# Performance work log

Measured on AMD Instinct MI355X. Metric: run time of the kernel, lower is better.

Reference implementation:

```python
import jax, jax.numpy as jnp
import numpy as np

HIDDEN = 51
INPUT = 1
OUTPUT = 1
BATCH = 4096
SEQ = 999


def setup_inputs() -> dict:
    key = jax.random.key(0)
    ks = jax.random.split(key, 7)
    s = 1.0 / np.sqrt(HIDDEN)  # PyTorch default LSTM/Linear init scale
    u = lambda k, shape: jax.random.uniform(k, shape, jnp.float32, -s, s)
    return {
        "input": jax.random.normal(ks[0], (BATCH, SEQ, INPUT), jnp.float32),
        "W_ih": u(ks[1], (4 * HIDDEN, INPUT)),
        "W_hh": u(ks[2], (4 * HIDDEN, HIDDEN)),
        "b_ih": u(ks[3], (4 * HIDDEN,)),
        "b_hh": u(ks[4], (4 * HIDDEN,)),
        "W_fc": u(ks[5], (OUTPUT, HIDDEN)),
        "b_fc": u(ks[6], (OUTPUT,)),
        "future": 0,
    }


def reference(input, W_ih, W_hh, b_ih, b_hh, W_fc, b_fc, future):
    # Single-layer LSTM (PyTorch gate order i, f, g, o) scanned over time,
    # followed by a per-timestep Linear -> (batch, seq+future, output).
    def step(carry, x_t):
        h, c = carry
        gates = x_t @ W_ih.T + b_ih + h @ W_hh.T + b_hh  # (B, 4H)
        i, f, g, o = jnp.split(gates, 4, axis=-1)
        c = jax.nn.sigmoid(f) * c + jax.nn.sigmoid(i) * jnp.tanh(g)
        h = jax.nn.sigmoid(o) * jnp.tanh(c)
        return (h, c), h

    B = input.shape[0]
    h0 = jnp.zeros((B, HIDDEN), input.dtype)
    c0 = jnp.zeros((B, HIDDEN), input.dtype)
    xs = jnp.swapaxes(input, 0, 1)  # (T, B, I)
    (h, c), hs = jax.lax.scan(step, (h0, c0), xs)
    ys = hs @ W_fc.T + b_fc  # (T, B, O)

    # static Python int, so a trace-time loop is fine).
    y = ys[-1]
    extra = []
    for _ in range(future):
        (h, c), hn = step((h, c), y)
        y = hn @ W_fc.T + b_fc
        extra.append(y)
    if extra:
        ys = jnp.concatenate([ys, jnp.stack(extra, 0)], axis=0)
    return jnp.swapaxes(ys, 0, 1)  # (B, T+future, O)
```

## Files before the change

kernel.cpp:

```cpp
#include <hip/hip_runtime.h>
#include <hip/hip_bf16.h>

#define HID   51
#define MR    208
#define SEQT  999
#define CH    111
#define NCH   9
#define EPB   16
#define XST   17
#define NTH   448
#define BSTR  72

typedef __attribute__((ext_vector_type(8))) short  short8;
typedef __attribute__((ext_vector_type(4))) float  floatx4;

__global__ void prep_kernel(const float* __restrict__ W_hh,
                            const float* __restrict__ W_ih,
                            const float* __restrict__ W_fc,
                            __hip_bfloat16* __restrict__ A_ext)
{
    const float K1 = 1.442695040889f;
    int idx = blockIdx.x * blockDim.x + threadIdx.x;
    if (idx >= MR * 64) return;
    int r = idx >> 6, k = idx & 63;
    int u = r >> 2, gate = r & 3;
    float v = 0.f;
    if (r == 204) {
        if (k < HID) v = W_fc[k];
    } else if (u < HID) {
        float s = (gate == 2) ? (-2.f * K1) : (-K1);
        if (k < HID)      v = s * W_hh[(gate * HID + u) * HID + k];
        else if (k == 51) v = s * W_ih[gate * HID + u];
    }
    A_ext[idx] = __float2bfloat16(v);
}

__launch_bounds__(NTH)
__global__ void lstm_mfma_kernel(const float* __restrict__ x,
                                 const float* __restrict__ b_ih,
                                 const float* __restrict__ b_hh,
                                 const float* __restrict__ b_fc,
                                 const __hip_bfloat16* __restrict__ A_ext,
                                 float* __restrict__ out)
{
    __shared__ __hip_bfloat16 bcol[2][16 * BSTR];
    __shared__ float x_lds[(CH + 1) * XST];
    __shared__ float y_lds[CH * XST];

    const int tid  = threadIdx.x;
    const int w    = tid >> 6;
    const int lane = tid & 63;
    const int e    = lane & 15;
    const int g4   = lane >> 4;
    const int e0   = blockIdx.x * EPB;
    const bool w6  = (w == 6);
    const int  uB6   = 48 + g4;
    const bool yln   = w6 && (g4 == 3);
    const bool xsv   = w6 && (g4 == 0);
    const int  wrow6 = (uB6 < HID) ? uB6 : 63;

    const float K1  = 1.442695040889f;
    const float K2N = -2.885390081777f;

    short8  A0a = {0,0,0,0,0,0,0,0}, A1a = {0,0,0,0,0,0,0,0};
    short8  A0b = {0,0,0,0,0,0,0,0}, A1b = {0,0,0,0,0,0,0,0};
    floatx4 bqa = {0.f, 0.f, 0.f, 0.f}, bqb = {0.f, 0.f, 0.f, 0.f};
    float   csa = 0.f, csb = 0.f;
    int ua = 0, ub = 0;

    if (!w6) {
        int Ta = 2 * w, Tb = 2 * w + 1;
        ua = 4 * Ta + g4; ub = 4 * Tb + g4;
        int ma = Ta * 16 + e, mb = Tb * 16 + e;
        A0a = *(const short8*)&A_ext[ma * 64 + g4 * 8];
        A1a = *(const short8*)&A_ext[ma * 64 + 32 + g4 * 8];
        A0b = *(const short8*)&A_ext[mb * 64 + g4 * 8];
        A1b = *(const short8*)&A_ext[mb * 64 + 32 + g4 * 8];
#pragma unroll
        for (int gg = 0; gg < 4; ++gg) {
            float s = (gg == 2) ? (-2.f * K1) : (-K1);
            bqa[gg] = s * (b_ih[gg * HID + ua] + b_hh[gg * HID + ua]);
            bqb[gg] = s * (b_ih[gg * HID + ub] + b_hh[gg * HID + ub]);
        }
    } else {
        int m = 12 * 16 + e;
        A0a = *(const short8*)&A_ext[m * 64 + g4 * 8];
        A1a = *(const short8*)&A_ext[m * 64 + 32 + g4 * 8];
        if (uB6 < HID) {
#pragma unroll
            for (int gg = 0; gg < 4; ++gg) {
                float s = (gg == 2) ? (-2.f * K1) : (-K1);
                bqa[gg] = s * (b_ih[gg * HID + uB6] + b_hh[gg * HID + uB6]);
            }
        }
    }

    for (int i = tid; i < 16 * BSTR; i += NTH) {
        bcol[0][i] = __float2bfloat16(0.f);
        bcol[1][i] = __float2bfloat16(0.f);
    }
    __syncthreads();
    if (tid < EPB)
        bcol[0][tid * BSTR + 51] = __float2bfloat16(x[(size_t)(e0 + tid) * SEQT]);
    const float bfc = b_fc[0];

    __syncthreads();

    for (int tc = 0; tc < NCH; ++tc) {
        const int t0 = tc * CH;
        for (int i2 = tid; i2 < (CH + 1) * EPB; i2 += NTH) {
            int ee = i2 / (CH + 1), tt = i2 % (CH + 1);
            int t = t0 + tt;
            x_lds[tt * XST + ee] = (t < SEQT) ? x[(size_t)(e0 + ee) * SEQT + t] : 0.f;
        }
        __syncthreads();

        for (int tt = 0; tt < CH; ++tt) {
            const int t  = t0 + tt;
            const int rp = t & 1, wp = rp ^ 1;

            short8 B0 = *(const short8*)&bcol[rp][e * BSTR + g4 * 8];
            short8 B1 = *(const short8*)&bcol[rp][e * BSTR + 32 + g4 * 8];

            if (!w6) {
                floatx4 aa = __builtin_amdgcn_mfma_f32_16x16x32_bf16(A0a, B0, bqa, 0, 0, 0);
                floatx4 ab = __builtin_amdgcn_mfma_f32_16x16x32_bf16(A0b, B0, bqb, 0, 0, 0);
                aa = __builtin_amdgcn_mfma_f32_16x16x32_bf16(A1a, B1, aa, 0, 0, 0);
                ab = __builtin_amdgcn_mfma_f32_16x16x32_bf16(A1b, B1, ab, 0, 0, 0);

                float Eia = __builtin_amdgcn_exp2f(aa[0]);
                float Efa = __builtin_amdgcn_exp2f(aa[1]);
                float Ega = __builtin_amdgcn_exp2f(aa[2]);
                float Eoa = __builtin_amdgcn_exp2f(aa[3]);
                float Eib = __builtin_amdgcn_exp2f(ab[0]);
                float Efb = __builtin_amdgcn_exp2f(ab[1]);
                float Egb = __builtin_amdgcn_exp2f(ab[2]);
                float Eob = __builtin_amdgcn_exp2f(ab[3]);

                float sfa  = __builtin_amdgcn_rcpf(1.f + Efa);
                float sfb  = __builtin_amdgcn_rcpf(1.f + Efb);
                float Riga = __builtin_amdgcn_rcpf(fmaf(Eia, Ega, (Eia + Ega) + 1.f));
                float Rigb = __builtin_amdgcn_rcpf(fmaf(Eib, Egb, (Eib + Egb) + 1.f));
                csa = fmaf(sfa, csa, K2N * ((1.f - Ega) * Riga));
                csb = fmaf(sfb, csb, K2N * ((1.f - Egb) * Rigb));
                float Eca = __builtin_amdgcn_exp2f(csa);
                float Ecb = __builtin_amdgcn_exp2f(csb);
                float Roca = __builtin_amdgcn_rcpf(fmaf(Eoa, Eca, (Eoa + Eca) + 1.f));
                float Rocb = __builtin_amdgcn_rcpf(fmaf(Eob, Ecb, (Eob + Ecb) + 1.f));
                float ha = (1.f - Eca) * Roca;
                float hb = (1.f - Ecb) * Rocb;

                bcol[wp][e * BSTR + ua] = __float2bfloat16(ha);
                bcol[wp][e * BSTR + ub] = __float2bfloat16(hb);
            } else {
                floatx4 acc = __builtin_amdgcn_mfma_f32_16x16x32_bf16(A0a, B0, bqa, 0, 0, 0);
                acc = __builtin_amdgcn_mfma_f32_16x16x32_bf16(A1a, B1, acc, 0, 0, 0);

                float Ei = __builtin_amdgcn_exp2f(acc[0]);
                float Ef = __builtin_amdgcn_exp2f(acc[1]);
                float Eg = __builtin_amdgcn_exp2f(acc[2]);
                float Eo = __builtin_amdgcn_exp2f(acc[3]);
                float sf  = __builtin_amdgcn_rcpf(1.f + Ef);
                float Rig = __builtin_amdgcn_rcpf(fmaf(Ei, Eg, (Ei + Eg) + 1.f));
                csa = fmaf(sf, csa, K2N * ((1.f - Eg) * Rig));
                float Ec = __builtin_amdgcn_exp2f(csa);
                float Roc = __builtin_amdgcn_rcpf(fmaf(Eo, Ec, (Eo + Ec) + 1.f));
                float h = (1.f - Ec) * Roc;

                bcol[wp][e * BSTR + wrow6] = __float2bfloat16((uB6 < HID) ? h : 0.f);
                if (yln) y_lds[tt * XST + e] = acc[0] + bfc;
                if (xsv) bcol[wp][e * BSTR + 51] =
                             __float2bfloat16(x_lds[(tt + 1) * XST + e]);
            }

            __syncthreads();
        }
        __syncthreads();

        for (int i2 = tid; i2 < CH * EPB; i2 += NTH) {
            int ee = i2 / CH, tt = i2 % CH;
            int t = t0 + tt - 1;
            if (t >= 0)
                out[(size_t)(e0 + ee) * SEQT + t] = y_lds[tt * XST + ee];
        }
        __syncthreads();
    }

    if (w6) {
        short8 B0 = *(const short8*)&bcol[1][e * BSTR + g4 * 8];
        short8 B1 = *(const short8*)&bcol[1][e * BSTR + 32 + g4 * 8];
        floatx4 acc = __builtin_amdgcn_mfma_f32_16x16x32_bf16(A0a, B0, bqa, 0, 0, 0);
        acc = __builtin_amdgcn_mfma_f32_16x16x32_bf16(A1a, B1, acc, 0, 0, 0);
        if (g4 == 3)
            out[(size_t)(e0 + e) * SEQT + (SEQT - 1)] = acc[0] + bfc;
    }
}

extern "C" void kernel_launch(void* const* d_in, const int* in_sizes, int n_in,
                              void* d_out, int out_size, void* d_ws, size_t ws_size,
                              hipStream_t stream) {
    const float* x    = (const float*)d_in[0];
    const float* W_ih = (const float*)d_in[1];
    const float* W_hh = (const float*)d_in[2];
    const float* b_ih = (const float*)d_in[3];
    const float* b_hh = (const float*)d_in[4];
    const float* W_fc = (const float*)d_in[5];
    const float* b_fc = (const float*)d_in[6];
    float* out = (float*)d_out;

    __hip_bfloat16* A_ext = (__hip_bfloat16*)d_ws;

    prep_kernel<<<(MR * 64 + 255) / 256, 256, 0, stream>>>(W_hh, W_ih, W_fc, A_ext);
    lstm_mfma_kernel<<<4096 / EPB, NTH, 0, stream>>>(x, b_ih, b_hh,
                                                     b_fc, A_ext, out);
}
```

Baseline: 435.1 us.

## Spread gate tiles over 13 waves, one tile each, and merge cell-update reciprocals

Each block now runs 13 waves of one 16-row MFMA tile each, instead of 7 waves where 6 handled two tiles, so every wave executes identical code and the per-step serial chain per wave is shorter. The cell update is rewritten algebraically so the forget and input/gate reciprocals become a single reciprocal of their product. The aim is a shorter per-timestep critical path in this latency-bound recurrence. In exchange there are more waves per block, more costly barriers, and possibly fewer blocks resident per CU.

Result: slower. 498.5 us (+14.6%).

```diff
diff --git a/kernel.cpp b/kernel.cpp
--- a/kernel.cpp
+++ b/kernel.cpp
@@ -8,7 +8,7 @@
 #define NCH   9
 #define EPB   16
 #define XST   17
-#define NTH   448
+#define NTH   832
 #define BSTR  72
 
 typedef __attribute__((ext_vector_type(8))) short  short8;
@@ -53,45 +53,29 @@
     const int e    = lane & 15;
     const int g4   = lane >> 4;
     const int e0   = blockIdx.x * EPB;
-    const bool w6  = (w == 6);
-    const int  uB6   = 48 + g4;
-    const bool yln   = w6 && (g4 == 3);
-    const bool xsv   = w6 && (g4 == 0);
-    const int  wrow6 = (uB6 < HID) ? uB6 : 63;
+
+    const int  u    = 4 * w + g4;
+    const bool yln  = (u == 51);
+    const bool xsv  = (w == 12) && (g4 == 0);
+    const int  wrow = (u < HID) ? u : 63;
 
     const float K1  = 1.442695040889f;
     const float K2N = -2.885390081777f;
 
-    short8  A0a = {0,0,0,0,0,0,0,0}, A1a = {0,0,0,0,0,0,0,0};
-    short8  A0b = {0,0,0,0,0,0,0,0}, A1b = {0,0,0,0,0,0,0,0};
-    floatx4 bqa = {0.f, 0.f, 0.f, 0.f}, bqb = {0.f, 0.f, 0.f, 0.f};
-    float   csa = 0.f, csb = 0.f;
-    int ua = 0, ub = 0;
+    short8  A0, A1;
+    floatx4 bq = {0.f, 0.f, 0.f, 0.f};
+    float   cs = 0.f;
 
-    if (!w6) {
-        int Ta = 2 * w, Tb = 2 * w + 1;
-        ua = 4 * Ta + g4; ub = 4 * Tb + g4;
-        int ma = Ta * 16 + e, mb = Tb * 16 + e;
-        A0a = *(const short8*)&A_ext[ma * 64 + g4 * 8];
-        A1a = *(const short8*)&A_ext[ma * 64 + 32 + g4 * 8];
-        A0b = *(const short8*)&A_ext[mb * 64 + g4 * 8];
-        A1b = *(const short8*)&A_ext[mb * 64 + 32 + g4 * 8];
+    {
+        int m = w * 16 + e;
+        A0 = *(const short8*)&A_ext[m * 64 + g4 * 8];
+        A1 = *(const short8*)&A_ext[m * 64 + 32 + g4 * 8];
+    }
+    if (u < HID) {
 #pragma unroll
         for (int gg = 0; gg < 4; ++gg) {
             float s = (gg == 2) ? (-2.f * K1) : (-K1);
-            bqa[gg] = s * (b_ih[gg * HID + ua] + b_hh[gg * HID + ua]);
-            bqb[gg] = s * (b_ih[gg * HID + ub] + b_hh[gg * HID + ub]);
-        }
-    } else {
-        int m = 12 * 16 + e;
-        A0a = *(const short8*)&A_ext[m * 64 + g4 * 8];
-        A1a = *(const short8*)&A_ext[m * 64 + 32 + g4 * 8];
-        if (uB6 < HID) {
-#pragma unroll
-            for (int gg = 0; gg < 4; ++gg) {
-                float s = (gg == 2) ? (-2.f * K1) : (-K1);
-                bqa[gg] = s * (b_ih[gg * HID + uB6] + b_hh[gg * HID + uB6]);
-            }
+            bq[gg] = s * (b_ih[gg * HID + u] + b_hh[gg * HID + u]);
         }
     }
 
@@ -122,56 +106,27 @@
             short8 B0 = *(const short8*)&bcol[rp][e * BSTR + g4 * 8];
             short8 B1 = *(const short8*)&bcol[rp][e * BSTR + 32 + g4 * 8];
 
-            if (!w6) {
-                floatx4 aa = __builtin_amdgcn_mfma_f32_16x16x32_bf16(A0a, B0, bqa, 0, 0, 0);
-                floatx4 ab = __builtin_amdgcn_mfma_f32_16x16x32_bf16(A0b, B0, bqb, 0, 0, 0);
-                aa = __builtin_amdgcn_mfma_f32_16x16x32_bf16(A1a, B1, aa, 0, 0, 0);
-                ab = __builtin_amdgcn_mfma_f32_16x16x32_bf16(A1b, B1, ab, 0, 0, 0);
+            floatx4 acc = __builtin_amdgcn_mfma_f32_16x16x32_bf16(A0, B0, bq, 0, 0, 0);
+            acc = __builtin_amdgcn_mfma_f32_16x16x32_bf16(A1, B1, acc, 0, 0, 0);
 
-                float Eia = __builtin_amdgcn_exp2f(aa[0]);
-                float Efa = __builtin_amdgcn_exp2f(aa[1]);
-                float Ega = __builtin_amdgcn_exp2f(aa[2]);
-                float Eoa = __builtin_amdgcn_exp2f(aa[3]);
-                float Eib = __builtin_amdgcn_exp2f(ab[0]);
-                float Efb = __builtin_amdgcn_exp2f(ab[1]);
-                float Egb = __builtin_amdgcn_exp2f(ab[2]);
-                float Eob = __builtin_amdgcn_exp2f(ab[3]);
+            float Ei = __builtin_amdgcn_exp2f(acc[0]);
+            float Ef = __builtin_amdgcn_exp2f(acc[1]);
+            float Eg = __builtin_amdgcn_exp2f(acc[2]);
+            float Eo = __builtin_amdgcn_exp2f(acc[3]);
 
-                float sfa  = __builtin_amdgcn_rcpf(1.f + Efa);
-                float sfb  = __builtin_amdgcn_rcpf(1.f + Efb);
-                float Riga = __builtin_amdgcn_rcpf(fmaf(Eia, Ega, (Eia + Ega) + 1.f));
-                float Rigb = __builtin_amdgcn_rcpf(fmaf(Eib, Egb, (Eib + Egb) + 1.f));
-                csa = fmaf(sfa, csa, K2N * ((1.f - Ega) * Riga));
-                csb = fmaf(sfb, csb, K2N * ((1.f - Egb) * Rigb));
-                float Eca = __builtin_amdgcn_exp2f(csa);
-                float Ecb = __builtin_amdgcn_exp2f(csb);
-                float Roca = __builtin_amdgcn_rcpf(fmaf(Eoa, Eca, (Eoa + Eca) + 1.f));
-                float Rocb = __builtin_amdgcn_rcpf(fmaf(Eob, Ecb, (Eob + Ecb) + 1.f));
-                float ha = (1.f - Eca) * Roca;
-                float hb = (1.f - Ecb) * Rocb;
+            float P  = fmaf(Ei, Eg, (Ei + Eg) + 1.f);
+            float F1 = 1.f + Ef;
+            float R  = __builtin_amdgcn_rcpf(F1 * P);
+            cs = fmaf(cs, P, K2N * ((1.f - Eg) * F1)) * R;
 
-                bcol[wp][e * BSTR + ua] = __float2bfloat16(ha);
-                bcol[wp][e * BSTR + ub] = __float2bfloat16(hb);
-            } else {
-                floatx4 acc = __builtin_amdgcn_mfma_f32_16x16x32_bf16(A0a, B0, bqa, 0, 0, 0);
-                acc = __builtin_amdgcn_mfma_f32_16x16x32_bf16(A1a, B1, acc, 0, 0, 0);
+            float Ec  = __builtin_amdgcn_exp2f(cs);
+            float Roc = __builtin_amdgcn_rcpf(fmaf(Eo, Ec, (Eo + Ec) + 1.f));
+            float h   = (1.f - Ec) * Roc;
 
-                float Ei = __builtin_amdgcn_exp2f(acc[0]);
-                float Ef = __builtin_amdgcn_exp2f(acc[1]);
-                float Eg = __builtin_amdgcn_exp2f(acc[2]);
-                float Eo = __builtin_amdgcn_exp2f(acc[3]);
-                float sf  = __builtin_amdgcn_rcpf(1.f + Ef);
-                float Rig = __builtin_amdgcn_rcpf(fmaf(Ei, Eg, (Ei + Eg) + 1.f));
-                csa = fmaf(sf, csa, K2N * ((1.f - Eg) * Rig));
-                float Ec = __builtin_amdgcn_exp2f(csa);
-                float Roc = __builtin_amdgcn_rcpf(fmaf(Eo, Ec, (Eo + Ec) + 1.f));
-                float h = (1.f - Ec) * Roc;
-
-                bcol[wp][e * BSTR + wrow6] = __float2bfloat16((uB6 < HID) ? h : 0.f);
-                if (yln) y_lds[tt * XST + e] = acc[0] + bfc;
-                if (xsv) bcol[wp][e * BSTR + 51] =
-                             __float2bfloat16(x_lds[(tt + 1) * XST + e]);
-            }
+            bcol[wp][e * BSTR + wrow] = __float2bfloat16((u < HID) ? h : 0.f);
+            if (yln) y_lds[tt * XST + e] = acc[0] + bfc;
+            if (xsv) bcol[wp][e * BSTR + 51] =
+                         __float2bfloat16(x_lds[(tt + 1) * XST + e]);
 
             __syncthreads();
         }
@@ -186,11 +141,11 @@
         __syncthreads();
     }
 
-    if (w6) {
+    if (w == 12) {
         short8 B0 = *(const short8*)&bcol[1][e * BSTR + g4 * 8];
         short8 B1 = *(const short8*)&bcol[1][e * BSTR + 32 + g4 * 8];
-        floatx4 acc = __builtin_amdgcn_mfma_f32_16x16x32_bf16(A0a, B0, bqa, 0, 0, 0);
-        acc = __builtin_amdgcn_mfma_f32_16x16x32_bf16(A1a, B1, acc, 0, 0, 0);
+        floatx4 acc = __builtin_amdgcn_mfma_f32_16x16x32_bf16(A0, B0, bq, 0, 0, 0);
+        acc = __builtin_amdgcn_mfma_f32_16x16x32_bf16(A1, B1, acc, 0, 0, 0);
         if (g4 == 3)
             out[(size_t)(e0 + e) * SEQT + (SEQT - 1)] = acc[0] + bfc;
     }
```

## Prefetch x chunks into registers, split MFMA chains, fuse sigmoid reciprocals, pack h stores

Applied to the files above, without the earlier changes.

The next chunk of inputs is now loaded into registers while the current chunk's recurrence runs, then written to LDS, which removes a serialized load phase and one barrier per chunk. The two dependent MFMAs per tile are split into independent accumulations that are summed afterwards, shortening the critical latency chain. The forget-gate and input-gate reciprocals are merged into one rcp, and rows are remapped so each lane writes two adjacent h values as one packed bf16 store. Costs include extra registers for the prefetch and a fused reciprocal whose product could overflow in fp32.

After: 430.4 us. Within noise of the previous version (-1.1%).

```diff
diff --git a/kernel.cpp b/kernel.cpp
--- a/kernel.cpp
+++ b/kernel.cpp
@@ -23,14 +23,22 @@
     int idx = blockIdx.x * blockDim.x + threadIdx.x;
     if (idx >= MR * 64) return;
     int r = idx >> 6, k = idx & 63;
-    int u = r >> 2, gate = r & 3;
+    int T = r >> 4, r16 = r & 15, g4r = r16 >> 2, gate = r16 & 3;
     float v = 0.f;
-    if (r == 204) {
-        if (k < HID) v = W_fc[k];
-    } else if (u < HID) {
+    if (T < 12) {
+        int u = ((T >> 1) << 3) + 2 * g4r + (T & 1);
         float s = (gate == 2) ? (-2.f * K1) : (-K1);
         if (k < HID)      v = s * W_hh[(gate * HID + u) * HID + k];
         else if (k == 51) v = s * W_ih[gate * HID + u];
+    } else {
+        if (g4r < 3) {
+            int u = 48 + g4r;
+            float s = (gate == 2) ? (-2.f * K1) : (-K1);
+            if (k < HID)      v = s * W_hh[(gate * HID + u) * HID + k];
+            else if (k == 51) v = s * W_ih[gate * HID + u];
+        } else if (gate == 0) {
+            if (k < HID) v = W_fc[k];
+        }
     }
     A_ext[idx] = __float2bfloat16(v);
 }
@@ -61,16 +69,17 @@
 
     const float K1  = 1.442695040889f;
     const float K2N = -2.885390081777f;
+    const floatx4 z4 = {0.f, 0.f, 0.f, 0.f};
 
     short8  A0a = {0,0,0,0,0,0,0,0}, A1a = {0,0,0,0,0,0,0,0};
     short8  A0b = {0,0,0,0,0,0,0,0}, A1b = {0,0,0,0,0,0,0,0};
     floatx4 bqa = {0.f, 0.f, 0.f, 0.f}, bqb = {0.f, 0.f, 0.f, 0.f};
     float   csa = 0.f, csb = 0.f;
-    int ua = 0, ub = 0;
+    int ua = 0;
 
     if (!w6) {
         int Ta = 2 * w, Tb = 2 * w + 1;
-        ua = 4 * Ta + g4; ub = 4 * Tb + g4;
+        ua = 8 * w + 2 * g4;
         int ma = Ta * 16 + e, mb = Tb * 16 + e;
         A0a = *(const short8*)&A_ext[ma * 64 + g4 * 8];
         A1a = *(const short8*)&A_ext[ma * 64 + 32 + g4 * 8];
@@ -79,8 +88,8 @@
 #pragma unroll
         for (int gg = 0; gg < 4; ++gg) {
             float s = (gg == 2) ? (-2.f * K1) : (-K1);
-            bqa[gg] = s * (b_ih[gg * HID + ua] + b_hh[gg * HID + ua]);
-            bqb[gg] = s * (b_ih[gg * HID + ub] + b_hh[gg * HID + ub]);
+            bqa[gg] = s * (b_ih[gg * HID + ua]     + b_hh[gg * HID + ua]);
+            bqb[gg] = s * (b_ih[gg * HID + ua + 1] + b_hh[gg * HID + ua + 1]);
         }
     } else {
         int m = 12 * 16 + e;
@@ -102,18 +111,28 @@
     __syncthreads();
     if (tid < EPB)
         bcol[0][tid * BSTR + 51] = __float2bfloat16(x[(size_t)(e0 + tid) * SEQT]);
+    for (int i2 = tid; i2 < (CH + 1) * EPB; i2 += NTH) {
+        int ee = i2 / (CH + 1), tt = i2 % (CH + 1);
+        x_lds[tt * XST + ee] = x[(size_t)(e0 + ee) * SEQT + tt];
+    }
     const float bfc = b_fc[0];
 
     __syncthreads();
 
     for (int tc = 0; tc < NCH; ++tc) {
         const int t0 = tc * CH;
-        for (int i2 = tid; i2 < (CH + 1) * EPB; i2 += NTH) {
-            int ee = i2 / (CH + 1), tt = i2 % (CH + 1);
-            int t = t0 + tt;
-            x_lds[tt * XST + ee] = (t < SEQT) ? x[(size_t)(e0 + ee) * SEQT + t] : 0.f;
-        }
-        __syncthreads();
+
+        float xpre[4];
+        {
+            const int t0n = t0 + CH;
+#pragma unroll
+            for (int q = 0; q < 4; ++q) {
+                int i2 = tid + q * NTH;
+                int ee = i2 / (CH + 1), tt = i2 - ee * (CH + 1);
+                int t = t0n + tt;
+                xpre[q] = (t < SEQT) ? x[(size_t)(e0 + ee) * SEQT + t] : 0.f;
+            }
+        }
 
         for (int tt = 0; tt < CH; ++tt) {
             const int t  = t0 + tt;
@@ -124,25 +143,27 @@
 
             if (!w6) {
                 floatx4 aa = __builtin_amdgcn_mfma_f32_16x16x32_bf16(A0a, B0, bqa, 0, 0, 0);
+                floatx4 a2 = __builtin_amdgcn_mfma_f32_16x16x32_bf16(A1a, B1, z4,  0, 0, 0);
                 floatx4 ab = __builtin_amdgcn_mfma_f32_16x16x32_bf16(A0b, B0, bqb, 0, 0, 0);
-                aa = __builtin_amdgcn_mfma_f32_16x16x32_bf16(A1a, B1, aa, 0, 0, 0);
-                ab = __builtin_amdgcn_mfma_f32_16x16x32_bf16(A1b, B1, ab, 0, 0, 0);
-
-                float Eia = __builtin_amdgcn_exp2f(aa[0]);
-                float Efa = __builtin_amdgcn_exp2f(aa[1]);
-                float Ega = __builtin_amdgcn_exp2f(aa[2]);
-                float Eoa = __builtin_amdgcn_exp2f(aa[3]);
-                float Eib = __builtin_amdgcn_exp2f(ab[0]);
-                float Efb = __builtin_amdgcn_exp2f(ab[1]);
-                float Egb = __builtin_amdgcn_exp2f(ab[2]);
-                float Eob = __builtin_amdgcn_exp2f(ab[3]);
-
-                float sfa  = __builtin_amdgcn_rcpf(1.f + Efa);
-                float sfb  = __builtin_amdgcn_rcpf(1.f + Efb);
-                float Riga = __builtin_amdgcn_rcpf(fmaf(Eia, Ega, (Eia + Ega) + 1.f));
-                float Rigb = __builtin_amdgcn_rcpf(fmaf(Eib, Egb, (Eib + Egb) + 1.f));
-                csa = fmaf(sfa, csa, K2N * ((1.f - Ega) * Riga));
-                csb = fmaf(sfb, csb, K2N * ((1.f - Egb) * Rigb));
+                floatx4 b2 = __builtin_amdgcn_mfma_f32_16x16x32_bf16(A1b, B1, z4,  0, 0, 0);
+
+                float Eia = __builtin_amdgcn_exp2f(aa[0] + a2[0]);
+                float Efa = __builtin_amdgcn_exp2f(aa[1] + a2[1]);
+                float Ega = __builtin_amdgcn_exp2f(aa[2] + a2[2]);
+                float Eoa = __builtin_amdgcn_exp2f(aa[3] + a2[3]);
+                float Eib = __builtin_amdgcn_exp2f(ab[0] + b2[0]);
+                float Efb = __builtin_amdgcn_exp2f(ab[1] + b2[1]);
+                float Egb = __builtin_amdgcn_exp2f(ab[2] + b2[2]);
+                float Eob = __builtin_amdgcn_exp2f(ab[3] + b2[3]);
+
+                float Pa  = fmaf(Eia, Ega, (Eia + Ega) + 1.f);
+                float Pb  = fmaf(Eib, Egb, (Eib + Egb) + 1.f);
+                float F1a = 1.f + Efa;
+                float F1b = 1.f + Efb;
+                float Ra  = __builtin_amdgcn_rcpf(F1a * Pa);
+                float Rb  = __builtin_amdgcn_rcpf(F1b * Pb);
+                csa = fmaf(csa, Pa, K2N * ((1.f - Ega) * F1a)) * Ra;
+                csb = fmaf(csb, Pb, K2N * ((1.f - Egb) * F1b)) * Rb;
                 float Eca = __builtin_amdgcn_exp2f(csa);
                 float Ecb = __builtin_amdgcn_exp2f(csb);
                 float Roca = __builtin_amdgcn_rcpf(fmaf(Eoa, Eca, (Eoa + Eca) + 1.f));
@@ -150,38 +171,46 @@
                 float ha = (1.f - Eca) * Roca;
                 float hb = (1.f - Ecb) * Rocb;
 
-                bcol[wp][e * BSTR + ua] = __float2bfloat16(ha);
-                bcol[wp][e * BSTR + ub] = __float2bfloat16(hb);
+                unsigned hpk;
+                asm("v_cvt_pk_bf16_f32 %0, %1, %2" : "=v"(hpk) : "v"(ha), "v"(hb));
+                *(unsigned*)&bcol[wp][e * BSTR + ua] = hpk;
             } else {
                 floatx4 acc = __builtin_amdgcn_mfma_f32_16x16x32_bf16(A0a, B0, bqa, 0, 0, 0);
-                acc = __builtin_amdgcn_mfma_f32_16x16x32_bf16(A1a, B1, acc, 0, 0, 0);
-
-                float Ei = __builtin_amdgcn_exp2f(acc[0]);
-                float Ef = __builtin_amdgcn_exp2f(acc[1]);
-                float Eg = __builtin_amdgcn_exp2f(acc[2]);
-                float Eo = __builtin_amdgcn_exp2f(acc[3]);
-                float sf  = __builtin_amdgcn_rcpf(1.f + Ef);
-                float Rig = __builtin_amdgcn_rcpf(fmaf(Ei, Eg, (Ei + Eg) + 1.f));
-                csa = fmaf(sf, csa, K2N * ((1.f - Eg) * Rig));
-                float Ec = __builtin_amdgcn_exp2f(csa);
+                floatx4 ac2 = __builtin_amdgcn_mfma_f32_16x16x32_bf16(A1a, B1, z4,  0, 0, 0);
+
+                float s0 = acc[0] + ac2[0];
+                float Ei = __builtin_amdgcn_exp2f(s0);
+                float Ef = __builtin_amdgcn_exp2f(acc[1] + ac2[1]);
+                float Eg = __builtin_amdgcn_exp2f(acc[2] + ac2[2]);
+                float Eo = __builtin_amdgcn_exp2f(acc[3] + ac2[3]);
+                float P  = fmaf(Ei, Eg, (Ei + Eg) + 1.f);
+                float F1 = 1.f + Ef;
+                float R  = __builtin_amdgcn_rcpf(F1 * P);
+                csa = fmaf(csa, P, K2N * ((1.f - Eg) * F1)) * R;
+                float Ec  = __builtin_amdgcn_exp2f(csa);
                 float Roc = __builtin_amdgcn_rcpf(fmaf(Eo, Ec, (Eo + Ec) + 1.f));
-                float h = (1.f - Ec) * Roc;
+                float h   = (1.f - Ec) * Roc;
 
                 bcol[wp][e * BSTR + wrow6] = __float2bfloat16((uB6 < HID) ? h : 0.f);
-                if (yln) y_lds[tt * XST + e] = acc[0] + bfc;
+                if (yln) y_lds[tt * XST + e] = s0 + bfc;
                 if (xsv) bcol[wp][e * BSTR + 51] =
                              __float2bfloat16(x_lds[(tt + 1) * XST + e]);
             }
 
             __syncthreads();
         }
-        __syncthreads();
 
         for (int i2 = tid; i2 < CH * EPB; i2 += NTH) {
             int ee = i2 / CH, tt = i2 % CH;
             int t = t0 + tt - 1;
             if (t >= 0)
                 out[(size_t)(e0 + ee) * SEQT + t] = y_lds[tt * XST + ee];
+        }
+#pragma unroll
+        for (int q = 0; q < 4; ++q) {
+            int i2 = tid + q * NTH;
+            int ee = i2 / (CH + 1), tt = i2 - ee * (CH + 1);
+            x_lds[tt * XST + ee] = xpre[q];
         }
         __syncthreads();
     }
```
